# Kernel optimization log

Measured on AMD Instinct MI355X. Metric: run time of the kernel, lower is better.

Reference implementation:

```python
import jax, jax.numpy as jnp
import numpy as np


def setup_inputs() -> dict:
    key = jax.random.key(0)
    qkv = jax.random.normal(key, (2, 1536, 4096), dtype=jnp.float32)
    return {"qkv": qkv, "num_heads": 8}


def reference(qkv, num_heads):
    bs, width, length = qkv.shape
    ch = width // (3 * num_heads)
    # [B*H, 3*ch, T] -> split into q, k, v each [B*H, ch, T]
    qkv_h = qkv.reshape(bs * num_heads, 3 * ch, length)
    q, k, v = qkv_h[:, :ch], qkv_h[:, ch:2 * ch], qkv_h[:, 2 * ch:]
    scale = 1.0 / np.sqrt(np.sqrt(ch)).astype(np.float32)
    # scores: [B*H, T, T]
    weight = jnp.einsum('bct,bcs->bts', q * scale, k * scale)
    weight = jax.nn.softmax(weight.astype(jnp.float32), axis=-1).astype(weight.dtype)
    a = jnp.einsum('bts,bcs->bct', weight, v)  # [B*H, ch, T]
    return a.reshape(bs, num_heads * ch, length)
```

## Files before the change

### kernel.cpp

```cpp
#include <hip/hip_runtime.h>
#include <hip/hip_bf16.h>

typedef __bf16 bf16x8 __attribute__((ext_vector_type(8)));
typedef __bf16 bf16x4 __attribute__((ext_vector_type(4)));
typedef __bf16 bf16x2 __attribute__((ext_vector_type(2)));
typedef float  f32x4  __attribute__((ext_vector_type(4)));

#define T_LEN 4096
#define QBLK  128
#define NIT   32

__device__ __forceinline__ int swz(int row, int colByte) {
    return row * 128 + (colByte ^ (((row ^ (row >> 2)) & 7) << 4));
}
__device__ __forceinline__ int swzM(int row, int colByte) {
    return row * 128 + (colByte ^ ((row & 7) << 4));
}
__device__ __forceinline__ int swzO(int row, int colByte) {
    return row * 512 + (colByte ^ ((row & 7) << 5));
}

#define QSCALE 0.18033688011112042f

#if __has_builtin(__builtin_amdgcn_exp2f)
#define EXP2(x) __builtin_amdgcn_exp2f(x)
#else
__device__ __forceinline__ float EXP2(float x) {
    float r; asm("v_exp_f32 %0, %1" : "=v"(r) : "v"(x)); return r;
}
#endif

__device__ __forceinline__ void glds16(const void* g, void* l) {
    __builtin_amdgcn_global_load_lds(
        (const __attribute__((address_space(1))) void*)g,
        (__attribute__((address_space(3))) void*)l, 16, 0, 0);
}

__global__ __launch_bounds__(256)
void qkv_prepass(const float* __restrict__ qkv, char* __restrict__ kpan,
                 char* __restrict__ vpan) {
    const int tile = blockIdx.x;
    const int bh   = blockIdx.y;
    const float* kp = qkv + ((size_t)bh * 192 + 64)  * T_LEN + tile * 64;
    const float* vp = qkv + ((size_t)bh * 192 + 128) * T_LEN + tile * 64;
    char* kout = kpan + (size_t)(bh * 64 + tile) * 8192;
    char* vout = vpan + (size_t)(bh * 64 + tile) * 8192;

    const int t  = threadIdx.x;
    const int s  = t & 63;
    const int o4 = t >> 6;
    #pragma unroll
    for (int oo = 0; oo < 2; ++oo) {
        const int oct = o4 + oo * 4;
        bf16x8 v;
        #pragma unroll
        for (int j = 0; j < 8; ++j)
            v[j] = (__bf16)kp[(size_t)(oct * 8 + j) * T_LEN + s];
        *(bf16x8*)(kout + swz(s, oct * 16)) = v;
    }
    const int c = t & 63;
    #pragma unroll
    for (int p = 0; p < 4; ++p) {
        const int u = o4 * 4 + p;
        float4 f = *(const float4*)(vp + (size_t)c * T_LEN + u * 4);
        const int up = (u & 8) | ((u & 3) << 1) | ((u >> 2) & 1);
        bf16x4 hv;
        hv[0] = (__bf16)f.x; hv[1] = (__bf16)f.y;
        hv[2] = (__bf16)f.z; hv[3] = (__bf16)f.w;
        *(bf16x4*)(vout + swz(c, up * 8)) = hv;
    }
}

__global__ __launch_bounds__(512, 4)
void qkv_attn_glds(const float* __restrict__ qkv, float* __restrict__ out,
                   const char* __restrict__ kpan, const char* __restrict__ vpan) {
    __shared__ __align__(16) char lds[81920];

    const int fid   = (blockIdx.x & 7) * 64 + (blockIdx.x >> 3);
    const int bh    = fid >> 5;
    const int ttile = fid & 31;
    const float* qp = qkv + (size_t)bh * 192 * T_LEN;
    const char* kpb = kpan + (size_t)bh * 64 * 8192;
    const char* vpb = vpan + (size_t)bh * 64 * 8192;
    const int t0 = ttile * QBLK;

    const int tid  = threadIdx.x;
    const int wave = tid >> 6, lane = tid & 63;
    const int g = lane >> 4, i = lane & 15;
    const int tg = wave >> 1, half = wave & 1;

    glds16(kpb + tid * 16,        lds + 16384 + wave * 1024);
    glds16(kpb + 8192 + tid * 16, lds + 16384 + 8192 + wave * 1024);
    glds16(vpb + tid * 16,        lds + 49152 + wave * 1024);
    glds16(vpb + 8192 + tid * 16, lds + 49152 + 8192 + wave * 1024);

    {
        const int tq  = (tid & 31) * 4;
        const int cp8 = tid >> 5;
        #pragma unroll
        for (int hh = 0; hh < 2; ++hh) {
            const int cpair = cp8 + hh * 16;
            const float* base = qp + (size_t)(cpair * 2) * T_LEN + t0 + tq;
            float4 lo = *(const float4*)(base);
            float4 hi = *(const float4*)(base + T_LEN);
            bf16x2 v;
            v[0] = (__bf16)(lo.x * QSCALE); v[1] = (__bf16)(hi.x * QSCALE);
            *(bf16x2*)(lds + swz(tq + 0, cpair * 4)) = v;
            v[0] = (__bf16)(lo.y * QSCALE); v[1] = (__bf16)(hi.y * QSCALE);
            *(bf16x2*)(lds + swz(tq + 1, cpair * 4)) = v;
            v[0] = (__bf16)(lo.z * QSCALE); v[1] = (__bf16)(hi.z * QSCALE);
            *(bf16x2*)(lds + swz(tq + 2, cpair * 4)) = v;
            v[0] = (__bf16)(lo.w * QSCALE); v[1] = (__bf16)(hi.w * QSCALE);
            *(bf16x2*)(lds + swz(tq + 3, cpair * 4)) = v;
        }
    }
    __syncthreads();
    bf16x8 qreg[2][2];
    #pragma unroll
    for (int h = 0; h < 2; ++h)
        #pragma unroll
        for (int kk = 0; kk < 2; ++kk)
            qreg[h][kk] = *(const bf16x8*)(lds + swz(tg * 32 + h * 16 + i, kk * 64 + g * 16));

    f32x4 oacc[2][4];
    #pragma unroll
    for (int h = 0; h < 2; ++h)
        #pragma unroll
        for (int n = 0; n < 4; ++n) oacc[h][n] = (f32x4){0.f, 0.f, 0.f, 0.f};
    float l0 = 0.f, l1 = 0.f;

    for (int it = 0; it < NIT; ++it) {
        if (it + 1 < NIT) {
            const size_t off = (size_t)(2 * it + 2) * 8192;
            const int b = (it + 1) & 1;
            glds16(kpb + off + tid * 16,        lds + 16384 + b * 16384 + wave * 1024);
            glds16(kpb + off + 8192 + tid * 16, lds + 16384 + b * 16384 + 8192 + wave * 1024);
            glds16(vpb + off + tid * 16,        lds + 49152 + b * 16384 + wave * 1024);
            glds16(vpb + off + 8192 + tid * 16, lds + 49152 + b * 16384 + 8192 + wave * 1024);
        }
        char* KsB = lds + 16384 + (it & 1) * 16384;
        char* VsB = lds + 49152 + (it & 1) * 16384;

        f32x4 sacc[2][2][2];
        #pragma unroll
        for (int ta = 0; ta < 2; ++ta)
            #pragma unroll
            for (int h = 0; h < 2; ++h)
                #pragma unroll
                for (int mt = 0; mt < 2; ++mt) sacc[ta][h][mt] = (f32x4){0.f, 0.f, 0.f, 0.f};
        __builtin_amdgcn_s_setprio(1);
        #pragma unroll
        for (int ta = 0; ta < 2; ++ta)
            #pragma unroll
            for (int kk = 0; kk < 2; ++kk)
                #pragma unroll
                for (int mt = 0; mt < 2; ++mt) {
                    bf16x8 kf = *(const bf16x8*)(KsB + ta * 8192 + swz(half * 32 + mt * 16 + i, kk * 64 + g * 16));
                    sacc[ta][0][mt] = __builtin_amdgcn_mfma_f32_16x16x32_bf16(kf, qreg[0][kk], sacc[ta][0][mt], 0, 0, 0);
                    sacc[ta][1][mt] = __builtin_amdgcn_mfma_f32_16x16x32_bf16(kf, qreg[1][kk], sacc[ta][1][mt], 0, 0, 0);
                }
        __builtin_amdgcn_s_setprio(0);

        bf16x8 pa[2][2];
        #pragma unroll
        for (int ta = 0; ta < 2; ++ta)
            #pragma unroll
            for (int r = 0; r < 4; ++r) {
                float a0 = EXP2(sacc[ta][0][0][r]);
                float a1 = EXP2(sacc[ta][0][1][r]);
                l0 += a0 + a1;
                pa[ta][0][r] = (__bf16)a0; pa[ta][0][4 + r] = (__bf16)a1;
                float b0 = EXP2(sacc[ta][1][0][r]);
                float b1 = EXP2(sacc[ta][1][1][r]);
                l1 += b0 + b1;
                pa[ta][1][r] = (__bf16)b0; pa[ta][1][4 + r] = (__bf16)b1;
            }

        __builtin_amdgcn_s_setprio(1);
        #pragma unroll
        for (int ta = 0; ta < 2; ++ta)
            #pragma unroll
            for (int n = 0; n < 4; ++n) {
                bf16x8 bv = *(const bf16x8*)(VsB + ta * 8192 + swz(n * 16 + i, half * 64 + g * 16));
                oacc[0][n] = __builtin_amdgcn_mfma_f32_16x16x32_bf16(pa[ta][0], bv, oacc[0][n], 0, 0, 0);
                oacc[1][n] = __builtin_amdgcn_mfma_f32_16x16x32_bf16(pa[ta][1], bv, oacc[1][n], 0, 0, 0);
            }
        __builtin_amdgcn_s_setprio(0);
        __syncthreads();
    }
    l0 += __shfl_xor(l0, 16); l0 += __shfl_xor(l0, 32);
    l1 += __shfl_xor(l1, 16); l1 += __shfl_xor(l1, 32);

    char* mbase = lds + 16384 + tg * 8192;
    float* lbase = (float*)(lds);
    if (half == 1) {
        #pragma unroll
        for (int h = 0; h < 2; ++h)
            #pragma unroll
            for (int n = 0; n < 4; ++n)
                *(f32x4*)(mbase + swzM(n * 16 + i, h * 64 + g * 16)) = oacc[h][n];
        if (g == 0) { lbase[tg * 32 + i] = l0; lbase[tg * 32 + 16 + i] = l1; }
    }
    __syncthreads();
    if (half == 0) {
        #pragma unroll
        for (int h = 0; h < 2; ++h)
            #pragma unroll
            for (int n = 0; n < 4; ++n)
                oacc[h][n] += *(const f32x4*)(mbase + swzM(n * 16 + i, h * 64 + g * 16));
        l0 += lbase[tg * 32 + i];
        l1 += lbase[tg * 32 + 16 + i];
    }
    __syncthreads();
    if (half == 0) {
        #pragma unroll
        for (int h = 0; h < 2; ++h) {
            float invl = 1.0f / (h ? l1 : l0);
            #pragma unroll
            for (int reg = 0; reg < 4; ++reg) {
                float inv_r = __shfl(invl, g * 4 + reg);
                int t_loc = tg * 32 + h * 16 + g * 4 + reg;
                #pragma unroll
                for (int n = 0; n < 4; ++n) {
                    int c = n * 16 + i;
                    *(float*)(lds + swzO(c, t_loc * 4)) = oacc[h][n][reg] * inv_r;
                }
            }
        }
    }
    __syncthreads();
    #pragma unroll
    for (int it = 0; it < 4; ++it) {
        int idx = it * 512 + tid;
        int c   = idx >> 5;
        int seg = idx & 31;
        float4 u = *(const float4*)(lds + swzO(c, seg * 16));
        *(float4*)(out + (size_t)(bh * 64 + c) * T_LEN + t0 + seg * 4) = u;
    }
}

__global__ __launch_bounds__(256)
void simple_attn(const float* __restrict__ qkv, float* __restrict__ out) {
    const int wave = threadIdx.x >> 6;
    const int lane = threadIdx.x & 63;
    const int t  = blockIdx.x * 4 + wave;
    const int bh = blockIdx.y;
    const float* qp = qkv + (size_t)bh * 192 * T_LEN;
    const float* kp = qp + (size_t)64  * T_LEN;
    const float* vp = qp + (size_t)128 * T_LEN;
    const float qc = qp[(size_t)lane * T_LEN + t] * 0.125f;
    float m = -1e30f, l = 0.f, o = 0.f;
    for (int s = 0; s < T_LEN; ++s) {
        float prod = qc * kp[(size_t)lane * T_LEN + s];
        #pragma unroll
        for (int d = 1; d < 64; d <<= 1) prod += __shfl_xor(prod, d);
        const float nm   = fmaxf(m, prod);
        const float corr = __expf(m - nm);
        const float p    = __expf(prod - nm);
        l = l * corr + p;
        o = o * corr + p * vp[(size_t)lane * T_LEN + s];
        m = nm;
    }
    out[(size_t)(bh * 64 + lane) * T_LEN + t] = o / l;
}

extern "C" void kernel_launch(void* const* d_in, const int* in_sizes, int n_in,
                              void* d_out, int out_size, void* d_ws, size_t ws_size,
                              hipStream_t stream) {
    const float* qkv = (const float*)d_in[0];
    float* out = (float*)d_out;
    const size_t pan_bytes = (size_t)16 * 64 * 8192;
    if (ws_size >= 2 * pan_bytes) {
        char* kpan = (char*)d_ws;
        char* vpan = kpan + pan_bytes;
        qkv_prepass<<<dim3(64, 16), 256, 0, stream>>>(qkv, kpan, vpan);
        qkv_attn_glds<<<dim3(512), 512, 0, stream>>>(qkv, out, kpan, vpan);
    } else {
        simple_attn<<<dim3(T_LEN / 4, 16), 256, 0, stream>>>(qkv, out);
    }
}
```

Baseline: 89.09 us.

## Switch KV loop to 4-slot ring with two-tile-ahead prefetch and one barrier

The K/V tile loop now steps over 64 half-size tiles instead of 32 double tiles. It uses a 4-slot LDS ring buffer and issues global-to-LDS loads two tiles ahead. The end-of-iteration __syncthreads is replaced by a single s_waitcnt vmcnt plus s_barrier at the top of each iteration, so the load for tile t+2 is in flight while tile t is computed. This deepens prefetch and cuts barrier stalls, but doubles the number of barriers and shrinks the MFMA work done between them.

After: 90.53 us. About the same (+1.6%).

```diff
diff --git a/kernel.cpp b/kernel.cpp
--- a/kernel.cpp
+++ b/kernel.cpp
@@ -8,7 +8,7 @@
 
 #define T_LEN 4096
 #define QBLK  128
-#define NIT   32
+#define NT    64
 
 __device__ __forceinline__ int swz(int row, int colByte) {
     return row * 128 + (colByte ^ (((row ^ (row >> 2)) & 7) << 4));
@@ -90,8 +90,8 @@
     const int tg = wave >> 1, half = wave & 1;
 
     glds16(kpb + tid * 16,        lds + 16384 + wave * 1024);
+    glds16(vpb + tid * 16,        lds + 49152 + wave * 1024);
     glds16(kpb + 8192 + tid * 16, lds + 16384 + 8192 + wave * 1024);
-    glds16(vpb + tid * 16,        lds + 49152 + wave * 1024);
     glds16(vpb + 8192 + tid * 16, lds + 49152 + 8192 + wave * 1024);
 
     {
@@ -129,68 +129,63 @@
         for (int n = 0; n < 4; ++n) oacc[h][n] = (f32x4){0.f, 0.f, 0.f, 0.f};
     float l0 = 0.f, l1 = 0.f;
 
-    for (int it = 0; it < NIT; ++it) {
-        if (it + 1 < NIT) {
-            const size_t off = (size_t)(2 * it + 2) * 8192;
-            const int b = (it + 1) & 1;
-            glds16(kpb + off + tid * 16,        lds + 16384 + b * 16384 + wave * 1024);
-            glds16(kpb + off + 8192 + tid * 16, lds + 16384 + b * 16384 + 8192 + wave * 1024);
-            glds16(vpb + off + tid * 16,        lds + 49152 + b * 16384 + wave * 1024);
-            glds16(vpb + off + 8192 + tid * 16, lds + 49152 + b * 16384 + 8192 + wave * 1024);
-        }
-        char* KsB = lds + 16384 + (it & 1) * 16384;
-        char* VsB = lds + 49152 + (it & 1) * 16384;
-
-        f32x4 sacc[2][2][2];
-        #pragma unroll
-        for (int ta = 0; ta < 2; ++ta)
-            #pragma unroll
-            for (int h = 0; h < 2; ++h)
-                #pragma unroll
-                for (int mt = 0; mt < 2; ++mt) sacc[ta][h][mt] = (f32x4){0.f, 0.f, 0.f, 0.f};
+    for (int t = 0; t < NT; ++t) {
+        if (t + 2 < NT) {
+            const size_t off = (size_t)(t + 2) * 8192;
+            const int b = (t + 2) & 3;
+            glds16(kpb + off + tid * 16, lds + 16384 + b * 8192 + wave * 1024);
+            glds16(vpb + off + tid * 16, lds + 49152 + b * 8192 + wave * 1024);
+            asm volatile("s_waitcnt vmcnt(4)\n\ts_barrier" ::: "memory");
+        } else if (t + 2 == NT) {
+            asm volatile("s_waitcnt vmcnt(2)\n\ts_barrier" ::: "memory");
+        } else {
+            asm volatile("s_waitcnt vmcnt(0)\n\ts_barrier" ::: "memory");
+        }
+        char* KsR = lds + 16384 + (t & 3) * 8192;
+        char* VsR = lds + 49152 + (t & 3) * 8192;
+
+        f32x4 sacc[2][2];
+        #pragma unroll
+        for (int h = 0; h < 2; ++h)
+            #pragma unroll
+            for (int mt = 0; mt < 2; ++mt) sacc[h][mt] = (f32x4){0.f, 0.f, 0.f, 0.f};
         __builtin_amdgcn_s_setprio(1);
         #pragma unroll
-        for (int ta = 0; ta < 2; ++ta)
-            #pragma unroll
-            for (int kk = 0; kk < 2; ++kk)
-                #pragma unroll
-                for (int mt = 0; mt < 2; ++mt) {
-                    bf16x8 kf = *(const bf16x8*)(KsB + ta * 8192 + swz(half * 32 + mt * 16 + i, kk * 64 + g * 16));
-                    sacc[ta][0][mt] = __builtin_amdgcn_mfma_f32_16x16x32_bf16(kf, qreg[0][kk], sacc[ta][0][mt], 0, 0, 0);
-                    sacc[ta][1][mt] = __builtin_amdgcn_mfma_f32_16x16x32_bf16(kf, qreg[1][kk], sacc[ta][1][mt], 0, 0, 0);
-                }
-        __builtin_amdgcn_s_setprio(0);
-
-        bf16x8 pa[2][2];
-        #pragma unroll
-        for (int ta = 0; ta < 2; ++ta)
-            #pragma unroll
-            for (int r = 0; r < 4; ++r) {
-                float a0 = EXP2(sacc[ta][0][0][r]);
-                float a1 = EXP2(sacc[ta][0][1][r]);
-                l0 += a0 + a1;
-                pa[ta][0][r] = (__bf16)a0; pa[ta][0][4 + r] = (__bf16)a1;
-                float b0 = EXP2(sacc[ta][1][0][r]);
-                float b1 = EXP2(sacc[ta][1][1][r]);
-                l1 += b0 + b1;
-                pa[ta][1][r] = (__bf16)b0; pa[ta][1][4 + r] = (__bf16)b1;
-            }
-
-        __builtin_amdgcn_s_setprio(1);
-        #pragma unroll
-        for (int ta = 0; ta < 2; ++ta)
-            #pragma unroll
-            for (int n = 0; n < 4; ++n) {
-                bf16x8 bv = *(const bf16x8*)(VsB + ta * 8192 + swz(n * 16 + i, half * 64 + g * 16));
-                oacc[0][n] = __builtin_amdgcn_mfma_f32_16x16x32_bf16(pa[ta][0], bv, oacc[0][n], 0, 0, 0);
-                oacc[1][n] = __builtin_amdgcn_mfma_f32_16x16x32_bf16(pa[ta][1], bv, oacc[1][n], 0, 0, 0);
+        for (int kk = 0; kk < 2; ++kk)
+            #pragma unroll
+            for (int mt = 0; mt < 2; ++mt) {
+                bf16x8 kf = *(const bf16x8*)(KsR + swz(half * 32 + mt * 16 + i, kk * 64 + g * 16));
+                sacc[0][mt] = __builtin_amdgcn_mfma_f32_16x16x32_bf16(kf, qreg[0][kk], sacc[0][mt], 0, 0, 0);
+                sacc[1][mt] = __builtin_amdgcn_mfma_f32_16x16x32_bf16(kf, qreg[1][kk], sacc[1][mt], 0, 0, 0);
             }
         __builtin_amdgcn_s_setprio(0);
-        __syncthreads();
+
+        bf16x8 pa0, pa1;
+        #pragma unroll
+        for (int r = 0; r < 4; ++r) {
+            float a0 = EXP2(sacc[0][0][r]);
+            float a1 = EXP2(sacc[0][1][r]);
+            l0 += a0 + a1;
+            pa0[r] = (__bf16)a0; pa0[4 + r] = (__bf16)a1;
+            float b0 = EXP2(sacc[1][0][r]);
+            float b1 = EXP2(sacc[1][1][r]);
+            l1 += b0 + b1;
+            pa1[r] = (__bf16)b0; pa1[4 + r] = (__bf16)b1;
+        }
+
+        __builtin_amdgcn_s_setprio(1);
+        #pragma unroll
+        for (int n = 0; n < 4; ++n) {
+            bf16x8 bv = *(const bf16x8*)(VsR + swz(n * 16 + i, half * 64 + g * 16));
+            oacc[0][n] = __builtin_amdgcn_mfma_f32_16x16x32_bf16(pa0, bv, oacc[0][n], 0, 0, 0);
+            oacc[1][n] = __builtin_amdgcn_mfma_f32_16x16x32_bf16(pa1, bv, oacc[1][n], 0, 0, 0);
+        }
+        __builtin_amdgcn_s_setprio(0);
     }
     l0 += __shfl_xor(l0, 16); l0 += __shfl_xor(l0, 32);
     l1 += __shfl_xor(l1, 16); l1 += __shfl_xor(l1, 32);
 
+    __syncthreads();
     char* mbase = lds + 16384 + tg * 8192;
     float* lbase = (float*)(lds);
     if (half == 1) {
```
